# Kernel tuning notes

Hardware: AMD Instinct MI355X
Metric: run time of the kernel (lower is better)

## Reference

```python
import jax, jax.numpy as jnp
import numpy as np

F_DIM = 128
N_NODES = 2000
N_EDGES = 64000
BATCH = 4
NUM_NEG = 32
NUM_REL = 18
NUM_LAYERS = 3
NODE_RATIO = 0.1
AVG_DEG_LOG = float(np.log(33.0))  # PNA scaler constant (avg in-degree ~32); source used a ones(1) placeholder which yields inf
EPS_STD = 1e-5
NEG_BIG = -1e30


def setup_inputs() -> dict:
    key = jax.random.key(0)
    ks = jax.random.split(key, 24)
    F = F_DIM

    def W(k, fin, fout):
        return jax.random.normal(k, (fin, fout), jnp.float32) / np.float32(np.sqrt(fin))

    return {
        "h_index": jax.random.randint(ks[0], (BATCH, NUM_NEG), 0, N_NODES),
        "r_index": jax.random.randint(ks[1], (BATCH, NUM_NEG), 0, NUM_REL),
        "t_index": jax.random.randint(ks[2], (BATCH, NUM_NEG), 0, N_NODES),
        "hidden_states": jax.random.normal(ks[3], (BATCH, F), jnp.float32),
        "rel_hidden_states": jax.random.normal(ks[4], (BATCH, F), jnp.float32),
        "edge_index": jax.random.randint(ks[5], (2, N_EDGES), 0, N_NODES),
        "x": jax.random.normal(ks[6], (N_NODES, F), jnp.float32),
        "batch": jnp.zeros((N_NODES,), jnp.int32),
        "rel_table": jax.random.normal(ks[7], (2 * NUM_REL, F), jnp.float32) * 0.1,
        "Wl": W(ks[8], 2 * F, F), "bl": jnp.zeros((F,), jnp.float32),
        "W1": W(ks[9], F, F), "b1": jnp.zeros((F,), jnp.float32),
        "W2": W(ks[10], F, 1), "b2": jnp.zeros((1,), jnp.float32),
        "Wpre": jnp.stack([W(ks[11 + i], 2 * F, F) for i in range(NUM_LAYERS)]),
        "bpre": jnp.zeros((NUM_LAYERS, F), jnp.float32),
        "Wpost": jnp.stack([W(ks[14 + i], 13 * F, F) for i in range(NUM_LAYERS)]),
        "bpost": jnp.zeros((NUM_LAYERS, F), jnp.float32),
        "Wlin": jnp.stack([W(ks[17 + i], F, F) for i in range(NUM_LAYERS)]),
        "blin": jnp.zeros((NUM_LAYERS, F), jnp.float32),
    }


def _score(hidden, rel, Wl, bl, W1, b1, W2, b2):
    # ConditionedPNA.score: heur = Linear(cat[hidden, rel]); mlp(heur * hidden).squeeze(-1)
    heur = jnp.concatenate([hidden, rel], -1) @ Wl + bl
    z = heur * hidden
    z = jax.nn.relu(z @ W1 + b1)
    return (z @ W2 + b2)[..., 0]


def _pna_conv(xn, row, col, emask, Wpre, bpre, Wpost, bpost, Wlin, blin):
    # PyG PNAConv, towers=1, pre/post_layers=1, aggr=[mean,max,min,std], scalers=[id,amp,att].
    # Edge subset (topk-selected edges with degree_ratio=1.0) expressed as boolean mask emask.
    Nn = xn.shape[0]
    m = jnp.concatenate([xn[col], xn[row]], -1) @ Wpre + bpre  # [E, F] message = pre_nn(cat[x_i, x_j])
    w = emask.astype(xn.dtype)
    cnt = jax.ops.segment_sum(w, col, Nn)                       # in-degree of masked subgraph
    denom = jnp.maximum(cnt, 1.0)[:, None]
    mw = m * w[:, None]
    mean = jax.ops.segment_sum(mw, col, Nn) / denom
    mean2 = jax.ops.segment_sum(m * mw, col, Nn) / denom
    std = jnp.sqrt(jax.nn.relu(mean2 - mean * mean) + EPS_STD)
    has = cnt[:, None] > 0
    mx = jnp.where(has, jax.ops.segment_max(jnp.where(emask[:, None], m, NEG_BIG), col, Nn), 0.0)
    mn = jnp.where(has, jax.ops.segment_min(jnp.where(emask[:, None], m, -NEG_BIG), col, Nn), 0.0)
    agg = jnp.concatenate([mean, mx, mn, std], -1)              # [Nn, 4F]
    logd = jnp.log(jnp.maximum(cnt, 1.0) + 1.0)[:, None]
    out = jnp.concatenate([agg, agg * (logd / AVG_DEG_LOG), agg * (AVG_DEG_LOG / logd)], -1)  # [Nn, 12F]
    h = jnp.concatenate([xn, out], -1) @ Wpost + bpost          # post_nn on cat[x, out]
    return h @ Wlin + blin


def reference(h_index, r_index, t_index, hidden_states, rel_hidden_states, edge_index, x, batch,
              rel_table, Wl, bl, W1, b1, W2, b2, Wpre, bpre, Wpost, bpost, Wlin, blin):
    B = h_index.shape[0]
    N, F = x.shape
    # negative_sample_to_tail
    is_t = jnp.all(h_index == h_index[:, :1], axis=-1, keepdims=True)
    h_idx = jnp.where(is_t, h_index, t_index)
    t_idx = jnp.where(is_t, t_index, h_index)
    r_idx = jnp.where(is_t, r_index, r_index + NUM_REL)
    rel_emb = rel_table[r_idx[:, 0]]  # [B, F]
    # repeat_graph
    offsets = (jnp.arange(B) * N).astype(h_idx.dtype)
    row = (edge_index[0][None, :] + offsets[:, None]).reshape(-1)  # [B*E]
    col = (edge_index[1][None, :] + offsets[:, None]).reshape(-1)
    h_idx = h_idx + offsets[:, None]
    t_idx = t_idx + offsets[:, None]
    Nn = B * N
    # init_input_embeds (x zeroed, then t then h written)
    xr = jnp.zeros((Nn, F), x.dtype)
    xr = xr.at[t_idx[:, 0]].set(rel_hidden_states)
    xr = xr.at[h_idx[:, 0]].set(hidden_states)
    s0 = jnp.zeros((Nn,), x.dtype).at[h_idx[:, 0]].set(
        _score(hidden_states, rel_emb, Wl, bl, W1, b1, W2, b2))
    score = jnp.repeat(s0, N)  # faithful repeat_interleave -> length B*N*N
    rel_exp = jnp.repeat(rel_emb, N, axis=0)  # [B*N, F]
    cur = xr
    for l in range(NUM_LAYERS):
        # select_edges: topk nodes by score, keep edges whose source is selected (degree_ratio=1.0)
        k = int(NODE_RATIO * score.shape[0])
        _, top_idx = jax.lax.top_k(score, k)
        node_sel = jnp.zeros((score.shape[0],), jnp.bool_).at[top_idx].set(True)
        emask = node_sel[row]
        cur = cur + _pna_conv(cur, row, col, emask,
                              Wpre[l], bpre[l], Wpost[l], bpost[l], Wlin[l], blin[l])
        score = _score(cur, rel_exp, Wl, bl, W1, b1, W2, b2)  # [B*N]
    return score[t_idx]  # [B, num_neg]
```

## Files before the change

kernel.cpp:

```cpp
#include <hip/hip_runtime.h>

#define F 128
#define NNODE 2000
#define NEDGE 64000
#define NBATCH 4
#define NN 8000
#define NRELC 18
#define KTOP 800
#define AVGLOG 3.4965075614664802f
#define EPSSTD 1e-5f
#define NCHUNK 250


__global__ void k_init(float* __restrict__ cur, int* __restrict__ hist){
  int i = blockIdx.x*blockDim.x + threadIdx.x;
  int stride = gridDim.x*blockDim.x;
  for(int t=i;t<NN*F;t+=stride) cur[t]=0.f;
  for(int t=i;t<NCHUNK*NNODE;t+=stride) hist[t]=0;
}

__global__ void k_meta(const int* __restrict__ h_index, const int* __restrict__ r_index,
                       const int* __restrict__ t_index, const float* __restrict__ hidden,
                       const float* __restrict__ rel_hidden, const float* __restrict__ rel_table,
                       const float* __restrict__ Wl, const float* __restrict__ bl,
                       const float* __restrict__ W1, const float* __restrict__ b1,
                       const float* __restrict__ W2, const float* __restrict__ b2,
                       float* __restrict__ cur, unsigned char* __restrict__ sel,
                       int* __restrict__ meta_i, float* __restrict__ meta_f){
  __shared__ int sh_ist[NBATCH], sh_h0[NBATCH], sh_t0[NBATCH], sh_r0[NBATCH];
  __shared__ float sh_rel[NBATCH*F];
  __shared__ float sh_z[F], sh_zz[F];
  __shared__ float sh_sc[NBATCH];
  __shared__ int sh_excl;
  int tid = threadIdx.x;
  if(tid<NBATCH){
    int b=tid;
    int h00=h_index[b*32];
    int ist=1;
    for(int j=1;j<32;j++) if(h_index[b*32+j]!=h00) ist=0;
    sh_ist[b]=ist;
    sh_h0[b] = (ist ? h_index[b*32] : t_index[b*32]) + b*NNODE;
    sh_t0[b] = (ist ? t_index[b*32] : h_index[b*32]) + b*NNODE;
    sh_r0[b] = r_index[b*32] + (ist?0:NRELC);
  }
  __syncthreads();
  if(tid<NBATCH*32){
    int b=tid>>5;
    meta_i[16+tid] = (sh_ist[b] ? t_index[tid] : h_index[tid]) + b*NNODE;
  }
  for(int t=tid;t<NBATCH*F;t+=blockDim.x){
    int b=t>>7, f=t&127;
    float v = rel_table[sh_r0[b]*F+f];
    sh_rel[t]=v; meta_f[t]=v;
  }
  __syncthreads();
  for(int t=tid;t<NBATCH*F;t+=blockDim.x){
    int b=t>>7, f=t&127;
    float acc=0.f;
    for(int k=0;k<F;k++) acc += sh_rel[b*F+k]*Wl[(F+k)*F+f];
    meta_f[512+t]=acc;
  }
  __syncthreads();
  for(int b=0;b<NBATCH;b++){
    if(tid<F){
      float acc=0.f;
      for(int k=0;k<F;k++) acc += hidden[b*F+k]*Wl[k*F+tid];
      float heur = acc + meta_f[512+b*F+tid] + bl[tid];
      sh_z[tid] = heur*hidden[b*F+tid];
    }
    __syncthreads();
    if(tid<F){
      float acc=0.f;
      for(int k=0;k<F;k++) acc += sh_z[k]*W1[k*F+tid];
      acc += b1[tid];
      sh_zz[tid] = acc>0.f?acc:0.f;
    }
    __syncthreads();
    if(tid==0){
      float s=0.f;
      for(int k=0;k<F;k++) s += sh_zz[k]*W2[k];
      sh_sc[b] = s + b2[0];
      meta_f[1024+b]=sh_sc[b];
    }
    __syncthreads();
  }
  if(tid==0){
    sh_excl = (sh_h0[0]<4 && sh_sc[0]<0.f) ? sh_h0[0] : -1;
    meta_i[8]=sh_excl;
  }
  __syncthreads();
  int ex = sh_excl;
  for(int t=tid;t<NN;t+=blockDim.x)
    sel[t] = (ex>=0 && (t/NNODE)==ex) ? 0 : 1;
  for(int t=tid;t<NBATCH*F;t+=blockDim.x){
    int b=t>>7, f=t&127;
    cur[sh_t0[b]*F+f] = rel_hidden[t];
  }
  __syncthreads();
  for(int t=tid;t<NBATCH*F;t+=blockDim.x){
    int b=t>>7, f=t&127;
    cur[sh_h0[b]*F+f] = hidden[t];
  }
}

__global__ __launch_bounds__(256) void k_hist(const int* __restrict__ edge,
                                              int* __restrict__ hist, int* __restrict__ rank){
  __shared__ int dsts[256];
  int chunk = blockIdx.x;
  int tid = threadIdx.x;
  int e = chunk*256 + tid;
  int d = edge[NEDGE + e];
  dsts[tid] = d;
  __syncthreads();
  int before=0, after=0;
  #pragma unroll 8
  for(int t=0;t<256;t++){
    int dt = dsts[t];
    before += (dt==d) & (t<tid);
    after  += (dt==d) & (t>tid);
  }
  rank[e] = before;
  if(after==0) hist[chunk*NNODE + d] = before+1;
}

__global__ void k_chunkscan(int* __restrict__ hist, int* __restrict__ deg){
  int node = blockIdx.x*blockDim.x + threadIdx.x;
  if(node>=NNODE) return;
  int run=0;
  for(int c=0;c<NCHUNK;c++){
    int v = hist[c*NNODE+node];
    hist[c*NNODE+node] = run;
    run += v;
  }
  deg[node]=run;
}

__global__ void k_scan(const int* __restrict__ deg, int* __restrict__ csr_start){
  __shared__ int a[2048], b[2048];
  int tid=threadIdx.x;
  for(int i=tid;i<2048;i+=256) a[i] = (i<NNODE)? deg[i] : 0;
  __syncthreads();
  int* src=a; int* dst=b;
  for(int off=1; off<2048; off<<=1){
    for(int i=tid;i<2048;i+=256){
      int v = src[i];
      if(i>=off) v += src[i-off];
      dst[i]=v;
    }
    __syncthreads();
    int* t=src; src=dst; dst=t;
  }
  for(int i=tid;i<=NNODE;i+=256) csr_start[i] = (i==0)?0:src[i-1];
}

__global__ void k_scatter(const int* __restrict__ edge, const int* __restrict__ hist,
                          const int* __restrict__ rank, const int* __restrict__ csr_start,
                          int* __restrict__ csr_src){
  int e = blockIdx.x*blockDim.x + threadIdx.x;
  if(e<NEDGE){
    int d = edge[NEDGE+e];
    int pos = csr_start[d] + hist[(e>>8)*NNODE + d] + rank[e];
    csr_src[pos] = edge[e];
  }
}


__global__ void k_sel(const float* __restrict__ score, unsigned char* __restrict__ sel){
  __shared__ float s[NN];
  int tid=threadIdx.x;
  float4* s4 = (float4*)s;
  const float4* g4 = (const float4*)score;
  for(int i=tid;i<NN/4;i+=256) s4[i]=g4[i];
  __syncthreads();
  int node = blockIdx.x*32 + (tid>>3);
  int part = tid & 7;
  float si = s[node];
  int rank = 0;
  for(int q=part*(NN/32); q<(part+1)*(NN/32); q++){
    float4 v = s4[q];
    int j = q*4;
    rank += (v.x>si)||(v.x==si && j  <node);
    rank += (v.y>si)||(v.y==si && j+1<node);
    rank += (v.z>si)||(v.z==si && j+2<node);
    rank += (v.w>si)||(v.w==si && j+3<node);
  }
  for(int o=4;o;o>>=1) rank += __shfl_down(rank, o, 8);
  if(part==0) sel[node] = (rank < KTOP) ? 1 : 0;
}

#define BM 64
#define BN 32
#define BKK 32
template<int MODE>
__global__ __launch_bounds__(256) void k_gemm(
    const float* __restrict__ A, const float* __restrict__ W,
    const float* __restrict__ bias, float* __restrict__ out,
    const float* __restrict__ AGGp, const float* __restrict__ F1p,
    const float* __restrict__ F2p, const float* __restrict__ RBp,
    const float* __restrict__ CURp, int Ktot)
{
  __shared__ float As[BM][36];
  __shared__ float Bs[BKK][36];
  int tid=threadIdx.x;
  int r0 = blockIdx.x*BM;
  int nblk = blockIdx.y*BN;
  int m0 = (tid>>3)*2;
  int n0 = (tid&7)*4;
  int am = tid>>2, ak=(tid&3)*8;
  int brw = tid>>3, bc=(tid&7)*4;
  float acc[2][4]={};
  for(int k0=0;k0<Ktot;k0+=BKK){
    {
      int row=r0+am;
      const float* src; float mult=1.f;
      if(MODE==1){
        if(k0<F)         src = CURp + row*F   + k0;
        else if(k0<640)  src = AGGp + row*512 + (k0-F);
        else if(k0<1152){ src = AGGp + row*512 + (k0-640);  mult=F1p[row]; }
        else            { src = AGGp + row*512 + (k0-1152); mult=F2p[row]; }
      } else src = A + row*F + k0;
      float4 v0 = *(const float4*)(src+ak);
      float4 v1 = *(const float4*)(src+ak+4);
      if(MODE==1){
        v0.x*=mult; v0.y*=mult; v0.z*=mult; v0.w*=mult;
        v1.x*=mult; v1.y*=mult; v1.z*=mult; v1.w*=mult;
      }
      *(float4*)&As[am][ak]   = v0;
      *(float4*)&As[am][ak+4] = v1;
    }
    {
      int wr=k0+brw, wc=nblk+bc;
      if(MODE==0 && nblk>=F){ wr+=F; wc-=F; }
      *(float4*)&Bs[brw][bc] = *(const float4*)&W[wr*F+wc];
    }
    __syncthreads();
    #pragma unroll
    for(int k=0;k<BKK;k++){
      float a0=As[m0][k], a1=As[m0+1][k];
      float4 b=*(float4*)&Bs[k][n0];
      acc[0][0]+=a0*b.x; acc[0][1]+=a0*b.y; acc[0][2]+=a0*b.z; acc[0][3]+=a0*b.w;
      acc[1][0]+=a1*b.x; acc[1][1]+=a1*b.y; acc[1][2]+=a1*b.z; acc[1][3]+=a1*b.w;
    }
    __syncthreads();
  }
  #pragma unroll
  for(int i=0;i<2;i++){
    int rr=r0+m0+i;
    #pragma unroll
    for(int j=0;j<4;j++){
      int cc=nblk+n0+j;
      float v=acc[i][j];
      if(MODE==0){ if(cc<F) v+=bias[cc]; out[rr*256+cc]=v; }
      else if(MODE==1){ out[rr*F+cc]=v+bias[cc]; }
      else if(MODE==2){ out[rr*F+cc]=CURp[rr*F+cc]+(v+bias[cc]); }
      else if(MODE==3){ float h=v+bias[cc]+RBp[(rr/NNODE)*F+cc]; out[rr*F+cc]=h*CURp[rr*F+cc]; }
      else            { float h=v+bias[cc]; out[rr*F+cc]=h>0.f?h:0.f; }
    }
  }
}

__global__ void k_agg(const float* __restrict__ AB, const unsigned char* __restrict__ sel,
                      const int* __restrict__ csr_start, const int* __restrict__ csr_src,
                      float* __restrict__ AGGo, float* __restrict__ F1o, float* __restrict__ F2o){
  int node = blockIdx.x*4 + (threadIdx.x>>6);
  int lane = threadIdx.x&63;
  int b = node/NNODE;
  int nl = node - b*NNODE;
  int boff = b*NNODE;
  int e0=csr_start[nl], e1=csr_start[nl+1];
  int f0=lane*2;
  float2 c = *(const float2*)&AB[node*256 + f0];
  float s1x=0,s1y=0,s2x=0,s2y=0;
  float mxx=-3e38f,mxy=-3e38f,mnx=3e38f,mny=3e38f;
  int cnt=0;
  for(int base=e0;base<e1;base+=64){
    int nch = e1-base; if(nch>64) nch=64;
    int pack=-1;
    if(lane<nch){
      int sg = csr_src[base+lane]+boff;
      pack = sel[sg] ? sg : -1;
    }
    for(int t=0;t<nch;t++){
      int sg = __shfl(pack, t);
      if(sg>=0){
        float2 v = *(const float2*)&AB[sg*256 + F + f0];
        float ma = c.x+v.x, mb = c.y+v.y;
        s1x+=ma; s1y+=mb;
        s2x+=ma*ma; s2y+=mb*mb;
        mxx=fmaxf(mxx,ma); mxy=fmaxf(mxy,mb);
        mnx=fminf(mnx,ma); mny=fminf(mny,mb);
        cnt++;
      }
    }
  }
  float meanx,meany,stdx,stdy,mxox,mxoy,mnox,mnoy;
  if(cnt>0){
    float fc=(float)cnt;
    meanx=s1x/fc; meany=s1y/fc;
    float m2x=s2x/fc, m2y=s2y/fc;
    float vx=m2x-meanx*meanx; if(vx<0.f)vx=0.f;
    float vy=m2y-meany*meany; if(vy<0.f)vy=0.f;
    stdx=sqrtf(vx+EPSSTD); stdy=sqrtf(vy+EPSSTD);
    mxox=mxx; mxoy=mxy; mnox=mnx; mnoy=mny;
  } else {
    meanx=0.f; meany=0.f;
    stdx=sqrtf(EPSSTD); stdy=stdx;
    mxox=0.f; mxoy=0.f; mnox=0.f; mnoy=0.f;
  }
  float logd = logf(fmaxf((float)cnt,1.f)+1.f);
  float2 w0={meanx,meany}; *(float2*)&AGGo[node*512      +f0]=w0;
  float2 w1={mxox,mxoy};   *(float2*)&AGGo[node*512+F    +f0]=w1;
  float2 w2v={mnox,mnoy};  *(float2*)&AGGo[node*512+2*F  +f0]=w2v;
  float2 w3={stdx,stdy};   *(float2*)&AGGo[node*512+3*F  +f0]=w3;
  if(lane==0){ F1o[node]=logd/AVGLOG; F2o[node]=AVGLOG/logd; }
}

__global__ void k_w2(const float* __restrict__ ZZ, const float* __restrict__ W2,
                     const float* __restrict__ b2, float* __restrict__ score){
  int row = blockIdx.x*4 + (threadIdx.x>>6);
  int lane = threadIdx.x&63;
  float2 z = *(const float2*)&ZZ[row*F + lane*2];
  float p = z.x*W2[lane*2] + z.y*W2[lane*2+1];
  for(int o=32;o;o>>=1) p += __shfl_down(p,o);
  if(lane==0) score[row] = p + b2[0];
}

__global__ void k_gather(const float* __restrict__ score, const int* __restrict__ meta_i,
                         float* __restrict__ outp){
  int t = threadIdx.x;
  if(t<128) outp[t] = score[meta_i[16+t]];
}


extern "C" void kernel_launch(void* const* d_in, const int* in_sizes, int n_in,
                              void* d_out, int out_size, void* d_ws, size_t ws_size,
                              hipStream_t stream){
  const int*   h_index    = (const int*)d_in[0];
  const int*   r_index    = (const int*)d_in[1];
  const int*   t_index    = (const int*)d_in[2];
  const float* hidden     = (const float*)d_in[3];
  const float* rel_hidden = (const float*)d_in[4];
  const int*   edge       = (const int*)d_in[5];
  const float* rel_table  = (const float*)d_in[8];
  const float* Wl =(const float*)d_in[9];   const float* bl =(const float*)d_in[10];
  const float* W1 =(const float*)d_in[11];  const float* b1 =(const float*)d_in[12];
  const float* W2 =(const float*)d_in[13];  const float* b2 =(const float*)d_in[14];
  const float* Wpre =(const float*)d_in[15];  const float* bpre =(const float*)d_in[16];
  const float* Wpost=(const float*)d_in[17];  const float* bpost=(const float*)d_in[18];
  const float* Wlin =(const float*)d_in[19];  const float* blin =(const float*)d_in[20];

  char* ws=(char*)d_ws;
  size_t off=0;
  auto alloc=[&](size_t bytes)->char*{ char* p=ws+off; off=(off+bytes+255)&~(size_t)255; return p; };
  float* cur   =(float*)alloc((size_t)NN*F*4);
  float* AB    =(float*)alloc((size_t)NN*256*4);
  float* AGG   =(float*)alloc((size_t)NN*512*4);
  float* Hb    =(float*)alloc((size_t)NN*F*4);
  float* score =(float*)alloc((size_t)NN*4);
  float* F1b   =(float*)alloc((size_t)NN*4);
  float* F2b   =(float*)alloc((size_t)NN*4);
  float* meta_f=(float*)alloc(2048*4);
  int*   meta_i=(int*)alloc(256*4);
  int*   deg   =(int*)alloc(NNODE*4);
  int*   csr_start=(int*)alloc((NNODE+1)*4);
  int*   csr_src  =(int*)alloc((size_t)NEDGE*4);
  int*   hist  =(int*)alloc((size_t)NCHUNK*NNODE*4);
  int*   rank  =(int*)alloc((size_t)NEDGE*4);
  unsigned char* sel=(unsigned char*)alloc(NN);
  float* Zb  = AB;
  float* ZZb = AB + (size_t)NN*F;

  k_init<<<512,256,0,stream>>>(cur, hist);
  k_meta<<<1,256,0,stream>>>(h_index,r_index,t_index,hidden,rel_hidden,rel_table,
                             Wl,bl,W1,b1,W2,b2,cur,sel,meta_i,meta_f);
  k_hist<<<NCHUNK,256,0,stream>>>(edge, hist, rank);
  k_chunkscan<<<8,256,0,stream>>>(hist, deg);
  k_scan<<<1,256,0,stream>>>(deg, csr_start);
  k_scatter<<<250,256,0,stream>>>(edge, hist, rank, csr_start, csr_src);

  for(int l=0;l<3;l++){
    if(l) k_sel<<<250,256,0,stream>>>(score, sel);
    k_gemm<0><<<dim3(125,8),256,0,stream>>>(cur, Wpre+(size_t)l*256*F, bpre+l*F, AB,
                                            nullptr,nullptr,nullptr,nullptr,nullptr, F);
    k_agg<<<2000,256,0,stream>>>(AB, sel, csr_start, csr_src, AGG, F1b, F2b);
    k_gemm<1><<<dim3(125,4),256,0,stream>>>(nullptr, Wpost+(size_t)l*1664*F, bpost+l*F, Hb,
                                            AGG, F1b, F2b, nullptr, cur, 1664);
    k_gemm<2><<<dim3(125,4),256,0,stream>>>(Hb, Wlin+(size_t)l*F*F, blin+l*F, cur,
                                            nullptr,nullptr,nullptr,nullptr, cur, F);
    k_gemm<3><<<dim3(125,4),256,0,stream>>>(cur, Wl, bl, Zb,
                                            nullptr,nullptr,nullptr, meta_f+512, cur, F);
    k_gemm<4><<<dim3(125,4),256,0,stream>>>(Zb, W1, b1, ZZb,
                                            nullptr,nullptr,nullptr,nullptr,nullptr, F);
    k_w2<<<2000,256,0,stream>>>(ZZb, W2, b2, score);
  }
  k_gather<<<1,128,0,stream>>>(score, meta_i, (float*)d_out);
}
```

Baseline: 599.3 us.

## Fuse per-layer tail GEMMs into one kernel and retile GEMM with double buffering

Merges the Wlin residual, the Wl scoring, the W1 ReLU layer and the W2 dot product into a single k_tail kernel. Each block keeps its 32-row tile in shared memory across all four steps, which removes three launches and the global round trips for the intermediate Z/ZZ buffers. The generic GEMM is retiled to 32x128 tiles with 4x4 per-thread outputs, a transposed A tile and register-prefetch double buffering. The post GEMM now launches only 250 blocks, which may underfill the GPU's compute units.

```diff
diff --git a/kernel.cpp b/kernel.cpp
--- a/kernel.cpp
+++ b/kernel.cpp
@@ -188,74 +188,245 @@
   if(part==0) sel[node] = (rank < KTOP) ? 1 : 0;
 }
 
-#define BM 64
-#define BN 32
-#define BKK 32
 template<int MODE>
 __global__ __launch_bounds__(256) void k_gemm(
     const float* __restrict__ A, const float* __restrict__ W,
     const float* __restrict__ bias, float* __restrict__ out,
     const float* __restrict__ AGGp, const float* __restrict__ F1p,
-    const float* __restrict__ F2p, const float* __restrict__ RBp,
-    const float* __restrict__ CURp, int Ktot)
+    const float* __restrict__ F2p, const float* __restrict__ CURp, int Ktot)
 {
-  __shared__ float As[BM][36];
-  __shared__ float Bs[BKK][36];
-  int tid=threadIdx.x;
-  int r0 = blockIdx.x*BM;
-  int nblk = blockIdx.y*BN;
-  int m0 = (tid>>3)*2;
-  int n0 = (tid&7)*4;
-  int am = tid>>2, ak=(tid&3)*8;
-  int brw = tid>>3, bc=(tid&7)*4;
-  float acc[2][4]={};
-  for(int k0=0;k0<Ktot;k0+=BKK){
-    {
-      int row=r0+am;
-      const float* src; float mult=1.f;
-      if(MODE==1){
-        if(k0<F)         src = CURp + row*F   + k0;
-        else if(k0<640)  src = AGGp + row*512 + (k0-F);
-        else if(k0<1152){ src = AGGp + row*512 + (k0-640);  mult=F1p[row]; }
-        else            { src = AGGp + row*512 + (k0-1152); mult=F2p[row]; }
-      } else src = A + row*F + k0;
-      float4 v0 = *(const float4*)(src+ak);
-      float4 v1 = *(const float4*)(src+ak+4);
-      if(MODE==1){
-        v0.x*=mult; v0.y*=mult; v0.z*=mult; v0.w*=mult;
-        v1.x*=mult; v1.y*=mult; v1.z*=mult; v1.w*=mult;
+  __shared__ float As[2][32][34];
+  __shared__ float Bs[2][32][128];
+  int tid = threadIdx.x;
+  int r0 = blockIdx.x*32;
+  int nblk = blockIdx.y*128;
+  int tm4 = (tid>>5)*4;
+  int tn4 = (tid&31)*4;
+  int am  = tid>>3;
+  int ak4 = (tid&7)*4;
+  int bk  = (tid>>5)*4;
+  int bc  = (tid&31)*4;
+
+  float mul1=1.f, mul2=1.f;
+  if(MODE==1){ mul1 = F1p[r0+am]; mul2 = F2p[r0+am]; }
+
+  float4 pa; float pmult=1.f; float4 pb[4];
+  int nt = Ktot/32;
+
+  auto load_tile = [&](int t){
+    int k0 = t*32;
+    const float* src; float mult = 1.f;
+    if(MODE==1){
+      if(k0<F)          src = CURp + (size_t)(r0+am)*F   + k0;
+      else if(k0<640)   src = AGGp + (size_t)(r0+am)*512 + (k0-F);
+      else if(k0<1152){ src = AGGp + (size_t)(r0+am)*512 + (k0-640);  mult=mul1; }
+      else            { src = AGGp + (size_t)(r0+am)*512 + (k0-1152); mult=mul2; }
+    } else src = A + (size_t)(r0+am)*F + k0;
+    pa = *(const float4*)(src + ak4);
+    pmult = mult;
+    #pragma unroll
+    for(int jj=0;jj<4;jj++){
+      int wr = k0 + bk + jj, wc = nblk + bc;
+      if(MODE==0 && nblk>=F){ wr+=F; wc-=F; }
+      pb[jj] = *(const float4*)&W[(size_t)wr*F + wc];
+    }
+  };
+  auto store_tile = [&](int b){
+    float4 v = pa;
+    if(MODE==1){ v.x*=pmult; v.y*=pmult; v.z*=pmult; v.w*=pmult; }
+    As[b][ak4  ][am] = v.x;
+    As[b][ak4+1][am] = v.y;
+    As[b][ak4+2][am] = v.z;
+    As[b][ak4+3][am] = v.w;
+    #pragma unroll
+    for(int jj=0;jj<4;jj++)
+      *(float4*)&Bs[b][bk+jj][bc] = pb[jj];
+  };
+
+  float acc[4][4]={};
+  load_tile(0);
+  store_tile(0);
+  __syncthreads();
+  for(int t=0;t<nt;t++){
+    if(t+1<nt) load_tile(t+1);
+    int b = t&1;
+    #pragma unroll
+    for(int k=0;k<32;k++){
+      float2 alo = *(const float2*)&As[b][k][tm4];
+      float2 ahi = *(const float2*)&As[b][k][tm4+2];
+      float4 bv  = *(const float4*)&Bs[b][k][tn4];
+      float av[4] = {alo.x, alo.y, ahi.x, ahi.y};
+      #pragma unroll
+      for(int i=0;i<4;i++){
+        acc[i][0] += av[i]*bv.x;
+        acc[i][1] += av[i]*bv.y;
+        acc[i][2] += av[i]*bv.z;
+        acc[i][3] += av[i]*bv.w;
       }
-      *(float4*)&As[am][ak]   = v0;
-      *(float4*)&As[am][ak+4] = v1;
-    }
-    {
-      int wr=k0+brw, wc=nblk+bc;
-      if(MODE==0 && nblk>=F){ wr+=F; wc-=F; }
-      *(float4*)&Bs[brw][bc] = *(const float4*)&W[wr*F+wc];
-    }
-    __syncthreads();
-    #pragma unroll
-    for(int k=0;k<BKK;k++){
-      float a0=As[m0][k], a1=As[m0+1][k];
-      float4 b=*(float4*)&Bs[k][n0];
-      acc[0][0]+=a0*b.x; acc[0][1]+=a0*b.y; acc[0][2]+=a0*b.z; acc[0][3]+=a0*b.w;
-      acc[1][0]+=a1*b.x; acc[1][1]+=a1*b.y; acc[1][2]+=a1*b.z; acc[1][3]+=a1*b.w;
-    }
-    __syncthreads();
-  }
-  #pragma unroll
-  for(int i=0;i<2;i++){
-    int rr=r0+m0+i;
+    }
+    if(t+1<nt) store_tile((t+1)&1);
+    __syncthreads();
+  }
+
+  #pragma unroll
+  for(int i=0;i<4;i++){
+    int rr = r0 + tm4 + i;
     #pragma unroll
     for(int j=0;j<4;j++){
-      int cc=nblk+n0+j;
-      float v=acc[i][j];
-      if(MODE==0){ if(cc<F) v+=bias[cc]; out[rr*256+cc]=v; }
-      else if(MODE==1){ out[rr*F+cc]=v+bias[cc]; }
-      else if(MODE==2){ out[rr*F+cc]=CURp[rr*F+cc]+(v+bias[cc]); }
-      else if(MODE==3){ float h=v+bias[cc]+RBp[(rr/NNODE)*F+cc]; out[rr*F+cc]=h*CURp[rr*F+cc]; }
-      else            { float h=v+bias[cc]; out[rr*F+cc]=h>0.f?h:0.f; }
-    }
+      int cc = nblk + tn4 + j;
+      float v = acc[i][j];
+      if(MODE==0){ if(cc<F) v+=bias[cc]; out[(size_t)rr*256+cc]=v; }
+      else       { out[(size_t)rr*F+cc]=v+bias[cc]; }
+    }
+  }
+}
+
+__global__ __launch_bounds__(256) void k_tail(
+    const float* __restrict__ Hb, float* __restrict__ cur,
+    const float* __restrict__ Wlin, const float* __restrict__ blin,
+    const float* __restrict__ Wl, const float* __restrict__ bl,
+    const float* __restrict__ W1, const float* __restrict__ b1,
+    const float* __restrict__ W2, const float* __restrict__ b2,
+    const float* __restrict__ RB, float* __restrict__ score)
+{
+  __shared__ float At [128][34];
+  __shared__ float At2[128][34];
+  __shared__ float Bs [32][128];
+  int tid = threadIdx.x;
+  int r0 = blockIdx.x*32;
+  int tm4 = (tid>>5)*4;
+  int tn4 = (tid&31)*4;
+  int am  = tid>>3;
+  int ak4 = (tid&7)*4;
+  int bk  = (tid>>5)*4;
+  int bc  = (tid&31)*4;
+
+  #pragma unroll
+  for(int kb=0;kb<4;kb++){
+    float4 v = *(const float4*)&Hb[(size_t)(r0+am)*F + kb*32 + ak4];
+    At[kb*32+ak4  ][am] = v.x;
+    At[kb*32+ak4+1][am] = v.y;
+    At[kb*32+ak4+2][am] = v.z;
+    At[kb*32+ak4+3][am] = v.w;
+  }
+  __syncthreads();
+
+  float acc[4][4];
+
+  #pragma unroll
+  for(int i=0;i<4;i++) for(int j=0;j<4;j++) acc[i][j]=0.f;
+  for(int kt=0;kt<4;kt++){
+    #pragma unroll
+    for(int jj=0;jj<4;jj++)
+      *(float4*)&Bs[bk+jj][bc] = *(const float4*)&Wlin[(size_t)(kt*32+bk+jj)*F + bc];
+    __syncthreads();
+    #pragma unroll
+    for(int k=0;k<32;k++){
+      float2 alo = *(const float2*)&At[kt*32+k][tm4];
+      float2 ahi = *(const float2*)&At[kt*32+k][tm4+2];
+      float4 bv  = *(const float4*)&Bs[k][tn4];
+      float av[4] = {alo.x, alo.y, ahi.x, ahi.y};
+      #pragma unroll
+      for(int i=0;i<4;i++){
+        acc[i][0]+=av[i]*bv.x; acc[i][1]+=av[i]*bv.y;
+        acc[i][2]+=av[i]*bv.z; acc[i][3]+=av[i]*bv.w;
+      }
+    }
+    __syncthreads();
+  }
+  #pragma unroll
+  for(int i=0;i<4;i++){
+    int rr = r0 + tm4 + i;
+    float4 c4 = *(const float4*)&cur[(size_t)rr*F + tn4];
+    float cv[4] = {c4.x, c4.y, c4.z, c4.w};
+    float ov[4];
+    #pragma unroll
+    for(int j=0;j<4;j++){
+      int cc = tn4 + j;
+      float val = cv[j] + (acc[i][j] + blin[cc]);
+      ov[j] = val;
+      At2[cc][tm4+i] = val;
+    }
+    float4 o4 = {ov[0],ov[1],ov[2],ov[3]};
+    *(float4*)&cur[(size_t)rr*F + tn4] = o4;
+  }
+  __syncthreads();
+
+  #pragma unroll
+  for(int i=0;i<4;i++) for(int j=0;j<4;j++) acc[i][j]=0.f;
+  for(int kt=0;kt<4;kt++){
+    #pragma unroll
+    for(int jj=0;jj<4;jj++)
+      *(float4*)&Bs[bk+jj][bc] = *(const float4*)&Wl[(size_t)(kt*32+bk+jj)*F + bc];
+    __syncthreads();
+    #pragma unroll
+    for(int k=0;k<32;k++){
+      float2 alo = *(const float2*)&At2[kt*32+k][tm4];
+      float2 ahi = *(const float2*)&At2[kt*32+k][tm4+2];
+      float4 bv  = *(const float4*)&Bs[k][tn4];
+      float av[4] = {alo.x, alo.y, ahi.x, ahi.y};
+      #pragma unroll
+      for(int i=0;i<4;i++){
+        acc[i][0]+=av[i]*bv.x; acc[i][1]+=av[i]*bv.y;
+        acc[i][2]+=av[i]*bv.z; acc[i][3]+=av[i]*bv.w;
+      }
+    }
+    __syncthreads();
+  }
+  #pragma unroll
+  for(int i=0;i<4;i++){
+    int rr = r0 + tm4 + i;
+    int bidx = rr/NNODE;
+    #pragma unroll
+    for(int j=0;j<4;j++){
+      int cc = tn4 + j;
+      float h = acc[i][j] + bl[cc] + RB[bidx*F+cc];
+      float z = h * At2[cc][tm4+i];
+      At[cc][tm4+i] = z;
+    }
+  }
+  __syncthreads();
+
+  #pragma unroll
+  for(int i=0;i<4;i++) for(int j=0;j<4;j++) acc[i][j]=0.f;
+  for(int kt=0;kt<4;kt++){
+    #pragma unroll
+    for(int jj=0;jj<4;jj++)
+      *(float4*)&Bs[bk+jj][bc] = *(const float4*)&W1[(size_t)(kt*32+bk+jj)*F + bc];
+    __syncthreads();
+    #pragma unroll
+    for(int k=0;k<32;k++){
+      float2 alo = *(const float2*)&At[kt*32+k][tm4];
+      float2 ahi = *(const float2*)&At[kt*32+k][tm4+2];
+      float4 bv  = *(const float4*)&Bs[k][tn4];
+      float av[4] = {alo.x, alo.y, ahi.x, ahi.y};
+      #pragma unroll
+      for(int i=0;i<4;i++){
+        acc[i][0]+=av[i]*bv.x; acc[i][1]+=av[i]*bv.y;
+        acc[i][2]+=av[i]*bv.z; acc[i][3]+=av[i]*bv.w;
+      }
+    }
+    __syncthreads();
+  }
+  #pragma unroll
+  for(int i=0;i<4;i++){
+    #pragma unroll
+    for(int j=0;j<4;j++){
+      int cc = tn4 + j;
+      float h = acc[i][j] + b1[cc];
+      At2[cc][tm4+i] = h>0.f ? h : 0.f;
+    }
+  }
+  __syncthreads();
+
+  int wv = tid>>6, ln = tid&63;
+  for(int r8=0;r8<8;r8++){
+    int r = wv*8 + r8;
+    float zx = At2[2*ln  ][r];
+    float zy = At2[2*ln+1][r];
+    float p = zx*W2[ln*2] + zy*W2[ln*2+1];
+    for(int o=32;o;o>>=1) p += __shfl_down(p,o);
+    if(ln==0) score[r0+r] = p + b2[0];
   }
 }
 
@@ -269,7 +440,7 @@
   int boff = b*NNODE;
   int e0=csr_start[nl], e1=csr_start[nl+1];
   int f0=lane*2;
-  float2 c = *(const float2*)&AB[node*256 + f0];
+  float2 c = *(const float2*)&AB[(size_t)node*256 + f0];
   float s1x=0,s1y=0,s2x=0,s2y=0;
   float mxx=-3e38f,mxy=-3e38f,mnx=3e38f,mny=3e38f;
   int cnt=0;
@@ -283,7 +454,7 @@
     for(int t=0;t<nch;t++){
       int sg = __shfl(pack, t);
       if(sg>=0){
-        float2 v = *(const float2*)&AB[sg*256 + F + f0];
+        float2 v = *(const float2*)&AB[(size_t)sg*256 + F + f0];
         float ma = c.x+v.x, mb = c.y+v.y;
         s1x+=ma; s1y+=mb;
         s2x+=ma*ma; s2y+=mb*mb;
@@ -308,21 +479,11 @@
     mxox=0.f; mxoy=0.f; mnox=0.f; mnoy=0.f;
   }
   float logd = logf(fmaxf((float)cnt,1.f)+1.f);
-  float2 w0={meanx,meany}; *(float2*)&AGGo[node*512      +f0]=w0;
-  float2 w1={mxox,mxoy};   *(float2*)&AGGo[node*512+F    +f0]=w1;
-  float2 w2v={mnox,mnoy};  *(float2*)&AGGo[node*512+2*F  +f0]=w2v;
-  float2 w3={stdx,stdy};   *(float2*)&AGGo[node*512+3*F  +f0]=w3;
+  float2 w0={meanx,meany}; *(float2*)&AGGo[(size_t)node*512      +f0]=w0;
+  float2 w1={mxox,mxoy};   *(float2*)&AGGo[(size_t)node*512+F    +f0]=w1;
+  float2 w2v={mnox,mnoy};  *(float2*)&AGGo[(size_t)node*512+2*F  +f0]=w2v;
+  float2 w3={stdx,stdy};   *(float2*)&AGGo[(size_t)node*512+3*F  +f0]=w3;
   if(lane==0){ F1o[node]=logd/AVGLOG; F2o[node]=AVGLOG/logd; }
-}
-
-__global__ void k_w2(const float* __restrict__ ZZ, const float* __restrict__ W2,
-                     const float* __restrict__ b2, float* __restrict__ score){
-  int row = blockIdx.x*4 + (threadIdx.x>>6);
-  int lane = threadIdx.x&63;
-  float2 z = *(const float2*)&ZZ[row*F + lane*2];
-  float p = z.x*W2[lane*2] + z.y*W2[lane*2+1];
-  for(int o=32;o;o>>=1) p += __shfl_down(p,o);
-  if(lane==0) score[row] = p + b2[0];
 }
 
 __global__ void k_gather(const float* __restrict__ score, const int* __restrict__ meta_i,
@@ -367,8 +528,6 @@
   int*   hist  =(int*)alloc((size_t)NCHUNK*NNODE*4);
   int*   rank  =(int*)alloc((size_t)NEDGE*4);
   unsigned char* sel=(unsigned char*)alloc(NN);
-  float* Zb  = AB;
-  float* ZZb = AB + (size_t)NN*F;
 
   k_init<<<512,256,0,stream>>>(cur, hist);
   k_meta<<<1,256,0,stream>>>(h_index,r_index,t_index,hidden,rel_hidden,rel_table,
@@ -380,18 +539,13 @@
 
   for(int l=0;l<3;l++){
     if(l) k_sel<<<250,256,0,stream>>>(score, sel);
-    k_gemm<0><<<dim3(125,8),256,0,stream>>>(cur, Wpre+(size_t)l*256*F, bpre+l*F, AB,
-                                            nullptr,nullptr,nullptr,nullptr,nullptr, F);
+    k_gemm<0><<<dim3(250,2),256,0,stream>>>(cur, Wpre+(size_t)l*256*F, bpre+l*F, AB,
+                                            nullptr,nullptr,nullptr,nullptr, F);
     k_agg<<<2000,256,0,stream>>>(AB, sel, csr_start, csr_src, AGG, F1b, F2b);
-    k_gemm<1><<<dim3(125,4),256,0,stream>>>(nullptr, Wpost+(size_t)l*1664*F, bpost+l*F, Hb,
-                                            AGG, F1b, F2b, nullptr, cur, 1664);
-    k_gemm<2><<<dim3(125,4),256,0,stream>>>(Hb, Wlin+(size_t)l*F*F, blin+l*F, cur,
-                                            nullptr,nullptr,nullptr,nullptr, cur, F);
-    k_gemm<3><<<dim3(125,4),256,0,stream>>>(cur, Wl, bl, Zb,
-                                            nullptr,nullptr,nullptr, meta_f+512, cur, F);
-    k_gemm<4><<<dim3(125,4),256,0,stream>>>(Zb, W1, b1, ZZb,
-                                            nullptr,nullptr,nullptr,nullptr,nullptr, F);
-    k_w2<<<2000,256,0,stream>>>(ZZb, W2, b2, score);
+    k_gemm<1><<<dim3(250,1),256,0,stream>>>(nullptr, Wpost+(size_t)l*1664*F, bpost+l*F, Hb,
+                                            AGG, F1b, F2b, cur, 1664);
+    k_tail<<<250,256,0,stream>>>(Hb, cur, Wlin+(size_t)l*F*F, blin+l*F,
+                                 Wl, bl, W1, b1, W2, b2, meta_f+512, score);
   }
   k_gather<<<1,128,0,stream>>>(score, meta_i, (float*)d_out);
 }
```

After: 780.9 us. 1.3x slower.
